# Kernel tuning notes

Measured on AMD Instinct MI355X. Metric: run time of the kernel, lower is better.

## Reference

```python
import jax, jax.numpy as jnp
import numpy as np

NUM_GROUPS = 32
EPS = 1e-6


def group_norm(x, gamma, beta):
    # x: (b, c, h, w)
    b, c, h, w = x.shape
    xg = x.reshape(b, NUM_GROUPS, c // NUM_GROUPS, h, w)
    mean = xg.mean(axis=(2, 3, 4), keepdims=True)
    var = xg.var(axis=(2, 3, 4), keepdims=True)
    xn = (xg - mean) * jax.lax.rsqrt(var + EPS)
    xn = xn.reshape(b, c, h, w)
    return xn * gamma[None, :, None, None] + beta[None, :, None, None]


def conv1x1(x, w, bias):
    # x: (b, c_in, h, w), w: (c_out, c_in) -> (b, c_out, h, w)
    return jnp.einsum('oc,bchw->bohw', w, x) + bias[None, :, None, None]


def setup_inputs() -> dict:
    key = jax.random.key(0)
    ks = jax.random.split(key, 11)
    c = 512
    x = jax.random.normal(ks[0], (4, c, 64, 64), dtype=jnp.float32)
    s = 1.0 / np.sqrt(c)
    return {
        'x': x,
        'gamma': jnp.ones((c,), jnp.float32),
        'beta': jnp.zeros((c,), jnp.float32),
        'wq': jax.random.normal(ks[1], (c, c), jnp.float32) * s,
        'bq': jax.random.normal(ks[2], (c,), jnp.float32) * 0.01,
        'wk': jax.random.normal(ks[3], (c, c), jnp.float32) * s,
        'bk': jax.random.normal(ks[4], (c,), jnp.float32) * 0.01,
        'wv': jax.random.normal(ks[5], (c, c), jnp.float32) * s,
        'bv': jax.random.normal(ks[6], (c,), jnp.float32) * s,
        'wo': jax.random.normal(ks[7], (c, c), jnp.float32) * s,
        'bo': jax.random.normal(ks[8], (c,), jnp.float32) * 0.01,
    }


def reference(x, gamma, beta, wq, bq, wk, bk, wv, bv, wo, bo):
    b, c, h, w = x.shape
    scale = c ** (-0.5)
    xn = group_norm(x, gamma, beta)
    q = conv1x1(xn, wq, bq).reshape(b, c, h * w)
    k = conv1x1(xn, wk, bk).reshape(b, c, h * w)
    v = conv1x1(xn, wv, bv).reshape(b, c, h * w)
    attn = jnp.einsum('bci,bcj->bij', q, k) * scale  # (b, hw, hw)
    attn = jax.nn.softmax(attn, axis=2)
    out = jnp.einsum('bij,bcj->bci', attn, v).reshape(b, c, h, w)
    out = conv1x1(out, wo, bo)
    return x + out
```

## Files before the change

### kernel.cpp

```cpp
#include <hip/hip_runtime.h>

typedef _Float16 f16x8 __attribute__((ext_vector_type(8)));
typedef float f32x4 __attribute__((ext_vector_type(4)));
typedef unsigned short u16;
typedef unsigned short u16x8 __attribute__((ext_vector_type(8)));

__device__ __forceinline__ u16 f2h(float f) {
  union { _Float16 h; u16 u; } v; v.h = (_Float16)f; return v.u;
}
__device__ __forceinline__ float h2f(u16 u) {
  union { _Float16 h; u16 u; } v; v.u = u; return (float)v.h;
}

__device__ __forceinline__ void gload16(const u16* g, u16* l) {
  __builtin_amdgcn_global_load_lds((const __attribute__((address_space(1))) unsigned*)g,
                                   (__attribute__((address_space(3))) unsigned*)l, 16, 0, 0);
}

__global__ void cast4_k(const float* __restrict__ a0, const float* __restrict__ a1,
                        const float* __restrict__ a2, const float* __restrict__ a3,
                        u16* __restrict__ o) {
  const float* src = blockIdx.y == 0 ? a0 : blockIdx.y == 1 ? a1 : blockIdx.y == 2 ? a2 : a3;
  int i = blockIdx.x * 256 + threadIdx.x;
  o[(size_t)blockIdx.y * 262144 + i] = f2h(src[i]);
}

__global__ void gn_k(const float* __restrict__ x, const float* __restrict__ g_,
                     const float* __restrict__ b_, u16* __restrict__ xnt) {
  const int g = blockIdx.x, b = blockIdx.y;
  const float* xb = x + ((size_t)b * 512 + g * 16) * 4096;
  u16* ob = xnt + (size_t)b * 4096 * 512 + g * 16;
  const float4* x4 = (const float4*)xb;
  float s = 0.f, ss = 0.f;
  for (int i = threadIdx.x; i < 16384; i += 256) {
    float4 v = x4[i];
    s += v.x + v.y + v.z + v.w;
    ss += v.x * v.x + v.y * v.y + v.z * v.z + v.w * v.w;
  }
  #pragma unroll
  for (int o = 32; o; o >>= 1) { s += __shfl_down(s, o); ss += __shfl_down(ss, o); }
  __shared__ float rs[4], rss[4];
  if ((threadIdx.x & 63) == 0) { rs[threadIdx.x >> 6] = s; rss[threadIdx.x >> 6] = ss; }
  __syncthreads();
  s = rs[0] + rs[1] + rs[2] + rs[3];
  ss = rss[0] + rss[1] + rss[2] + rss[3];
  const float mean = s * (1.f / 65536.f);
  const float rstd = rsqrtf(ss * (1.f / 65536.f) - mean * mean + 1e-6f);
  __shared__ float tile[16 * 257];
  const int cc_w = threadIdx.x & 15;
  const float gam = g_[g * 16 + cc_w] * rstd;
  const float bet = b_[g * 16 + cc_w] - mean * gam;
  for (int s0 = 0; s0 < 4096; s0 += 256) {
    __syncthreads();
    #pragma unroll
    for (int cc = 0; cc < 16; ++cc)
      tile[cc * 257 + threadIdx.x] = xb[(size_t)cc * 4096 + s0 + threadIdx.x];
    __syncthreads();
    #pragma unroll
    for (int it = 0; it < 16; ++it) {
      int sl = it * 16 + (threadIdx.x >> 4);
      float v = tile[cc_w * 257 + sl] * gam + bet;
      ob[(size_t)(s0 + sl) * 512 + cc_w] = f2h(v);
    }
  }
}

__global__ void softmax_k(u16* __restrict__ S) {
  const size_t ro = ((size_t)blockIdx.y * 4096 + blockIdx.x) * 4096;
  u16x8* rv = (u16x8*)(S + ro);
  const int tid = threadIdx.x;
  u16x8 h[2];
  h[0] = rv[tid];
  h[1] = rv[256 + tid];
  float v[16];
  #pragma unroll
  for (int t = 0; t < 2; ++t)
    #pragma unroll
    for (int j = 0; j < 8; ++j) v[t * 8 + j] = h2f(h[t][j]);
  float mx = -1e30f;
  #pragma unroll
  for (int i = 0; i < 16; ++i) mx = fmaxf(mx, v[i]);
  #pragma unroll
  for (int o = 32; o; o >>= 1) mx = fmaxf(mx, __shfl_down(mx, o));
  __shared__ float rm[4], rsu[4];
  if ((tid & 63) == 0) rm[tid >> 6] = mx;
  __syncthreads();
  mx = fmaxf(fmaxf(rm[0], rm[1]), fmaxf(rm[2], rm[3]));
  float sum = 0.f;
  #pragma unroll
  for (int i = 0; i < 16; ++i) { v[i] = __expf(v[i] - mx); sum += v[i]; }
  #pragma unroll
  for (int o = 32; o; o >>= 1) sum += __shfl_down(sum, o);
  if ((tid & 63) == 0) rsu[tid >> 6] = sum;
  __syncthreads();
  const float rinv = 1.f / (rsu[0] + rsu[1] + rsu[2] + rsu[3]);
  #pragma unroll
  for (int t = 0; t < 2; ++t) {
    u16x8 o8;
    #pragma unroll
    for (int j = 0; j < 8; ++j) o8[j] = f2h(v[t * 8 + j] * rinv);
    rv[t * 256 + tid] = o8;
  }
}

template<int MODE, int BM, int BN>
__global__ void gemm_k(const u16* __restrict__ A, int lda, long long sAz,
                       const u16* __restrict__ B, int ldb, long long sBz,
                       void* __restrict__ Cp_, int ldc, long long sCz,
                       int K,
                       u16* __restrict__ Cq, u16* __restrict__ Ck, u16* __restrict__ Cvv,
                       const float* __restrict__ bq, const float* __restrict__ bk,
                       const float* __restrict__ bvp) {
  const unsigned gx = gridDim.x, gy = gridDim.y;
  const unsigned lin = (blockIdx.z * gy + blockIdx.y) * gx + blockIdx.x;
  const unsigned nwg = gx * gy * gridDim.z;
  const unsigned swz = (lin & 7) * (nwg >> 3) + (lin >> 3);
  const unsigned bx = swz % gx;
  const unsigned rem = swz / gx;
  const unsigned by = rem % gy;
  const unsigned bz = rem / gy;

  constexpr int LK = 64;
  __shared__ u16 As[BM * LK];
  __shared__ u16 Bs[BN * LK];
  const int tid = threadIdx.x;
  const int m0 = by * BM;
  const int n0 = bx * BN;

  const u16* Ab;
  const u16* Bb;
  if constexpr (MODE == 5) {
    int proj = bz >> 2, b = bz & 3;
    Ab = A + (size_t)proj * 512 * 512;
    Bb = B + (size_t)b * 4096 * 512;
  } else {
    Ab = A + (size_t)bz * sAz;
    Bb = B + (size_t)bz * sBz;
  }

  constexpr int FM = BM / 32, FN = BN / 32;
  f32x4 acc[FM][FN];
  #pragma unroll
  for (int i = 0; i < FM; ++i)
    #pragma unroll
    for (int j = 0; j < FN; ++j)
      acc[i][j] = (f32x4){0.f, 0.f, 0.f, 0.f};

  const int wid = tid >> 6;
  const int lane = tid & 63;
  const int wm = (wid >> 1) * (BM / 2);
  const int wn = (wid & 1) * (BN / 2);
  const int l15 = lane & 15;
  const int lk8 = (lane >> 4) * 8;
  const int lrow = lane >> 3;
  const int lcol = (lane & 7) * 8;

  constexpr int ACH = BM / 8;
  constexpr int BCH = BN / 8;

  for (int k0 = 0; k0 < K; k0 += 64) {
    #pragma unroll
    for (int c = 0; c < ACH / 4; ++c) {
      int ch = wid * (ACH / 4) + c;
      gload16(Ab + (size_t)(m0 + ch * 8 + lrow) * lda + k0 + lcol, &As[ch * 512]);
    }
    #pragma unroll
    for (int c = 0; c < BCH / 4; ++c) {
      int ch = wid * (BCH / 4) + c;
      gload16(Bb + (size_t)(n0 + ch * 8 + lrow) * ldb + k0 + lcol, &Bs[ch * 512]);
    }
    __syncthreads();
    #pragma unroll
    for (int kk = 0; kk < 64; kk += 32) {
      f16x8 af[FM], bfr[FN];
      #pragma unroll
      for (int i = 0; i < FM; ++i)
        af[i] = *(const f16x8*)&As[(wm + i * 16 + l15) * LK + kk + lk8];
      #pragma unroll
      for (int j = 0; j < FN; ++j)
        bfr[j] = *(const f16x8*)&Bs[(wn + j * 16 + l15) * LK + kk + lk8];
      #pragma unroll
      for (int i = 0; i < FM; ++i)
        #pragma unroll
        for (int j = 0; j < FN; ++j)
          acc[i][j] = __builtin_amdgcn_mfma_f32_16x16x32_f16(af[i], bfr[j], acc[i][j], 0, 0, 0);
    }
    __syncthreads();
  }

  const int lq4 = (lane >> 4) * 4;
  if constexpr (MODE == 5) {
    int proj = bz >> 2, b = bz & 3;
    const float* bs = proj == 0 ? bq : (proj == 1 ? bk : bvp);
    u16* C = (proj == 0 ? Cq : (proj == 1 ? Ck : Cvv)) + (size_t)b * 4096 * 512;
    #pragma unroll
    for (int i = 0; i < FM; ++i) {
      int mb = m0 + wm + i * 16 + lq4;
      float b0 = bs[mb], b1 = bs[mb + 1], b2 = bs[mb + 2], b3 = bs[mb + 3];
      #pragma unroll
      for (int j = 0; j < FN; ++j) {
        int n = n0 + wn + j * 16 + l15;
        ushort4 o4;
        o4.x = f2h(acc[i][j][0] + b0); o4.y = f2h(acc[i][j][1] + b1);
        o4.z = f2h(acc[i][j][2] + b2); o4.w = f2h(acc[i][j][3] + b3);
        *(ushort4*)(C + (size_t)n * 512 + mb) = o4;
      }
    }
    return;
  }
  u16* C = (u16*)Cp_ + (size_t)bz * sCz;
  #pragma unroll
  for (int i = 0; i < FM; ++i) {
    int mb = m0 + wm + i * 16 + lq4;
    #pragma unroll
    for (int j = 0; j < FN; ++j) {
      int n = n0 + wn + j * 16 + l15;
      #pragma unroll
      for (int r = 0; r < 4; ++r)
        C[(size_t)(mb + r) * ldc + n] = f2h(acc[i][j][r]);
    }
  }
}

template<int BM, int BN, int EPI>
__global__ __launch_bounds__(512, 2)
void gemm8_k(const u16* __restrict__ A, int lda, long long sAz,
             const u16* __restrict__ B, int ldb, long long sBz,
             void* __restrict__ Cp_, int ldc, long long sCz,
             int K,
             const float* __restrict__ bias,
             const float* __restrict__ resid, long long sRz,
             float scale) {
  const unsigned gx = gridDim.x, gy = gridDim.y;
  const unsigned lin = (blockIdx.z * gy + blockIdx.y) * gx + blockIdx.x;
  const unsigned nwg = gx * gy * gridDim.z;
  const unsigned swzb = (lin & 7) * (nwg >> 3) + (lin >> 3);
  const unsigned bx = swzb % gx;
  const unsigned rem = swzb / gx;
  const unsigned by = rem % gy;
  const unsigned bz = rem / gy;

  constexpr int ACH = BM / 64;
  constexpr int BCH = BN / 64;
  constexpr int NLD = ACH + BCH;
  constexpr int HBUF = (BM + BN) * 64;
  __shared__ u16 lds[2 * HBUF];

  const int tid = threadIdx.x;
  const int m0 = by * BM;
  const int n0 = bx * BN;
  const u16* Ab = A + (size_t)bz * sAz + (size_t)m0 * lda;
  const u16* Bb = B + (size_t)bz * sBz + (size_t)n0 * ldb;

  int offA[ACH], offB[BCH];
  #pragma unroll
  for (int i = 0; i < ACH; ++i) {
    int ch = i * 512 + tid;
    int row = ch >> 3;
    int c16 = (ch & 7) ^ (row & 7);
    offA[i] = row * lda + c16 * 8;
  }
  #pragma unroll
  for (int i = 0; i < BCH; ++i) {
    int ch = i * 512 + tid;
    int row = ch >> 3;
    int c16 = (ch & 7) ^ (row & 7);
    offB[i] = row * ldb + c16 * 8;
  }

  const int wid = tid >> 6;
  const int lane = tid & 63;
  const int wm = (wid >> 2) * (BM / 2);
  const int wn = (wid & 3) * (BN / 4);
  const int l15 = lane & 15;
  const int lk8 = (lane >> 4) * 8;

  constexpr int FM = BM / 32;
  constexpr int FN = BN / 64;
  f32x4 acc[FM][FN];
  #pragma unroll
  for (int i = 0; i < FM; ++i)
    #pragma unroll
    for (int j = 0; j < FN; ++j)
      acc[i][j] = (f32x4){0.f, 0.f, 0.f, 0.f};

  const int NT = K >> 6;

  auto stage = [&](int t) {
    u16* dst = &lds[(t & 1) * HBUF];
    const u16* as = Ab + t * 64;
    #pragma unroll
    for (int i = 0; i < ACH; ++i)
      gload16(as + offA[i], dst + (i * 512 + tid) * 8);
    const u16* bs = Bb + t * 64;
    u16* dstB = dst + BM * 64;
    #pragma unroll
    for (int i = 0; i < BCH; ++i)
      gload16(bs + offB[i], dstB + (i * 512 + tid) * 8);
  };

  stage(0);
  stage(1);

  for (int t = 0; t < NT; ++t) {
    if (t < NT - 1)
      asm volatile("s_waitcnt vmcnt(%0)" :: "i"(NLD) : "memory");
    else
      asm volatile("s_waitcnt vmcnt(0)" ::: "memory");
    __builtin_amdgcn_s_barrier();
    __builtin_amdgcn_sched_barrier(0);

    const u16* Asp = &lds[(t & 1) * HBUF];
    const u16* Bsp = Asp + BM * 64;

    f16x8 bf[2][FN];
    #pragma unroll
    for (int k2 = 0; k2 < 2; ++k2)
      #pragma unroll
      for (int j = 0; j < FN; ++j) {
        int row = wn + j * 16 + l15;
        int col = (k2 * 32 + lk8) ^ ((row & 7) << 3);
        bf[k2][j] = *(const f16x8*)&Bsp[row * 64 + col];
      }
    #pragma unroll
    for (int q = 0; q < FM / 2; ++q) {
      f16x8 af[2][2];
      #pragma unroll
      for (int k2 = 0; k2 < 2; ++k2)
        #pragma unroll
        for (int s = 0; s < 2; ++s) {
          int row = wm + (2 * q + s) * 16 + l15;
          int col = (k2 * 32 + lk8) ^ ((row & 7) << 3);
          af[k2][s] = *(const f16x8*)&Asp[row * 64 + col];
        }
      __builtin_amdgcn_s_setprio(1);
      #pragma unroll
      for (int k2 = 0; k2 < 2; ++k2)
        #pragma unroll
        for (int s = 0; s < 2; ++s)
          #pragma unroll
          for (int j = 0; j < FN; ++j)
            acc[2 * q + s][j] =
                __builtin_amdgcn_mfma_f32_16x16x32_f16(af[k2][s], bf[k2][j], acc[2 * q + s][j], 0, 0, 0);
      __builtin_amdgcn_s_setprio(0);
    }

    asm volatile("s_waitcnt lgkmcnt(0)" ::: "memory");
    __builtin_amdgcn_sched_barrier(0);
    __builtin_amdgcn_s_barrier();
    if (t + 2 < NT) stage(t + 2);
  }

  const int lq4 = (lane >> 4) * 4;
  #pragma unroll
  for (int i = 0; i < FM; ++i) {
    int mb = m0 + wm + i * 16 + lq4;
    #pragma unroll
    for (int j = 0; j < FN; ++j) {
      int n = n0 + wn + j * 16 + l15;
      if constexpr (EPI == 0) {
        u16* C = (u16*)Cp_ + (size_t)bz * sCz;
        #pragma unroll
        for (int r = 0; r < 4; ++r)
          C[(size_t)(mb + r) * ldc + n] = f2h(acc[i][j][r] * scale);
      } else {
        float* C = (float*)Cp_ + (size_t)bz * sCz;
        const float* R = resid + (size_t)bz * sRz;
        #pragma unroll
        for (int r = 0; r < 4; ++r)
          C[(size_t)(mb + r) * ldc + n] = acc[i][j][r] + bias[mb + r] + R[(size_t)(mb + r) * ldc + n];
      }
    }
  }
}

extern "C" void kernel_launch(void* const* d_in, const int* in_sizes, int n_in,
                              void* d_out, int out_size, void* d_ws, size_t ws_size,
                              hipStream_t stream) {
  const float* x     = (const float*)d_in[0];
  const float* gamma = (const float*)d_in[1];
  const float* beta  = (const float*)d_in[2];
  const float* wq    = (const float*)d_in[3];
  const float* bq    = (const float*)d_in[4];
  const float* wk    = (const float*)d_in[5];
  const float* bk    = (const float*)d_in[6];
  const float* wv    = (const float*)d_in[7];
  const float* bv    = (const float*)d_in[8];
  const float* wo    = (const float*)d_in[9];
  const float* bo    = (const float*)d_in[10];
  float* out = (float*)d_out;

  const size_t BHW = (size_t)4096 * 512;
  const long long SS = 16777216LL;
  u16* Wh  = (u16*)d_ws;
  u16* xnt = Wh + (size_t)4 * 512 * 512;
  u16* qt  = xnt + 4 * BHW;
  u16* kt  = qt + 4 * BHW;
  u16* vt  = kt + 4 * BHW;
  u16* Sb  = vt + 4 * BHW;
  u16* Vp  = xnt;

  const float scale = 0.044194173824159216f;

  hipLaunchKernelGGL(cast4_k, dim3(1024, 4), dim3(256), 0, stream, wq, wk, wv, wo, Wh);
  hipLaunchKernelGGL(gn_k, dim3(32, 4), dim3(256), 0, stream, x, gamma, beta, xnt);

  hipLaunchKernelGGL((gemm_k<5, 128, 128>), dim3(32, 4, 12), dim3(256), 0, stream,
                     Wh, 512, 0LL, xnt, 512, 0LL, nullptr, 0, 0LL, 512,
                     qt, kt, vt, bq, bk, bv);

  hipLaunchKernelGGL((gemm8_k<256, 256, 0>), dim3(16, 16, 4), dim3(512), 0, stream,
                     qt, 512, (long long)BHW, kt, 512, (long long)BHW,
                     Sb, 4096, SS, 512, nullptr, nullptr, 0LL, scale);

  hipLaunchKernelGGL(softmax_k, dim3(4096, 4), dim3(256), 0, stream, Sb);

  hipLaunchKernelGGL((gemm_k<4, 128, 128>), dim3(32, 4, 4), dim3(256), 0, stream,
                     Wh + (size_t)3 * 512 * 512, 512, 0LL, vt, 512, (long long)BHW,
                     Vp, 4096, (long long)(512 * 4096), 512,
                     nullptr, nullptr, nullptr, nullptr, nullptr, nullptr);

  hipLaunchKernelGGL((gemm8_k<128, 256, 1>), dim3(16, 4, 4), dim3(512), 0, stream,
                     Vp, 4096, (long long)(512 * 4096), Sb, 4096, SS,
                     out, 4096, (long long)BHW, 4096, bo, x, (long long)BHW, 0.f);
}
```

Before: 408.5 us.

## Fuse softmax into QK^T epilogue with atomic row sums and deferred normalization

Drops the separate softmax kernel. The QK^T GEMM epilogue now exponentiates the scaled scores without subtracting a row max, clamping them to the fp16 range. It accumulates per-row sums with atomics into a zeroed buffer and stages the tile through LDS for vectorized stores. The final PV GEMM applies 1/rowsum per column in its epilogue, also through an LDS-staged coalesced path. This saves a full read and write of the 4096x4096 score matrix, but skipping the max subtraction risks overflow or precision loss for larger logits.

After: 452.6 us. 1.11x slower.

```diff
diff --git a/kernel.cpp b/kernel.cpp
--- a/kernel.cpp
+++ b/kernel.cpp
@@ -15,6 +15,10 @@
 __device__ __forceinline__ void gload16(const u16* g, u16* l) {
   __builtin_amdgcn_global_load_lds((const __attribute__((address_space(1))) unsigned*)g,
                                    (__attribute__((address_space(3))) unsigned*)l, 16, 0, 0);
+}
+
+__global__ void zero_k(float* __restrict__ p) {
+  p[blockIdx.x * 256 + threadIdx.x] = 0.f;
 }
 
 __global__ void cast4_k(const float* __restrict__ a0, const float* __restrict__ a1,
@@ -62,44 +66,6 @@
       float v = tile[cc_w * 257 + sl] * gam + bet;
       ob[(size_t)(s0 + sl) * 512 + cc_w] = f2h(v);
     }
-  }
-}
-
-__global__ void softmax_k(u16* __restrict__ S) {
-  const size_t ro = ((size_t)blockIdx.y * 4096 + blockIdx.x) * 4096;
-  u16x8* rv = (u16x8*)(S + ro);
-  const int tid = threadIdx.x;
-  u16x8 h[2];
-  h[0] = rv[tid];
-  h[1] = rv[256 + tid];
-  float v[16];
-  #pragma unroll
-  for (int t = 0; t < 2; ++t)
-    #pragma unroll
-    for (int j = 0; j < 8; ++j) v[t * 8 + j] = h2f(h[t][j]);
-  float mx = -1e30f;
-  #pragma unroll
-  for (int i = 0; i < 16; ++i) mx = fmaxf(mx, v[i]);
-  #pragma unroll
-  for (int o = 32; o; o >>= 1) mx = fmaxf(mx, __shfl_down(mx, o));
-  __shared__ float rm[4], rsu[4];
-  if ((tid & 63) == 0) rm[tid >> 6] = mx;
-  __syncthreads();
-  mx = fmaxf(fmaxf(rm[0], rm[1]), fmaxf(rm[2], rm[3]));
-  float sum = 0.f;
-  #pragma unroll
-  for (int i = 0; i < 16; ++i) { v[i] = __expf(v[i] - mx); sum += v[i]; }
-  #pragma unroll
-  for (int o = 32; o; o >>= 1) sum += __shfl_down(sum, o);
-  if ((tid & 63) == 0) rsu[tid >> 6] = sum;
-  __syncthreads();
-  const float rinv = 1.f / (rsu[0] + rsu[1] + rsu[2] + rsu[3]);
-  #pragma unroll
-  for (int t = 0; t < 2; ++t) {
-    u16x8 o8;
-    #pragma unroll
-    for (int j = 0; j < 8; ++j) o8[j] = f2h(v[t * 8 + j] * rinv);
-    rv[t * 256 + tid] = o8;
   }
 }
 
@@ -230,7 +196,7 @@
              int K,
              const float* __restrict__ bias,
              const float* __restrict__ resid, long long sRz,
-             float scale) {
+             float scale, float* __restrict__ rowsum) {
   const unsigned gx = gridDim.x, gy = gridDim.y;
   const unsigned lin = (blockIdx.z * gy + blockIdx.y) * gx + blockIdx.x;
   const unsigned nwg = gx * gy * gridDim.z;
@@ -244,7 +210,9 @@
   constexpr int BCH = BN / 64;
   constexpr int NLD = ACH + BCH;
   constexpr int HBUF = (BM + BN) * 64;
-  __shared__ u16 lds[2 * HBUF];
+  constexpr int EPIN = EPI == 1 ? BM * BN * 2 : BM * BN;
+  constexpr int LDSN = 2 * HBUF > EPIN ? 2 * HBUF : EPIN;
+  __shared__ u16 lds[LDSN];
 
   const int tid = threadIdx.x;
   const int m0 = by * BM;
@@ -352,24 +320,82 @@
   }
 
   const int lq4 = (lane >> 4) * 4;
-  #pragma unroll
-  for (int i = 0; i < FM; ++i) {
-    int mb = m0 + wm + i * 16 + lq4;
-    #pragma unroll
-    for (int j = 0; j < FN; ++j) {
-      int n = n0 + wn + j * 16 + l15;
-      if constexpr (EPI == 0) {
-        u16* C = (u16*)Cp_ + (size_t)bz * sCz;
+
+  if constexpr (EPI == 0) {
+    constexpr float L2E = 1.44269504088896f;
+    #pragma unroll
+    for (int i = 0; i < FM; ++i) {
+      #pragma unroll
+      for (int j = 0; j < FN; ++j)
         #pragma unroll
         for (int r = 0; r < 4; ++r)
-          C[(size_t)(mb + r) * ldc + n] = f2h(acc[i][j][r] * scale);
-      } else {
-        float* C = (float*)Cp_ + (size_t)bz * sCz;
-        const float* R = resid + (size_t)bz * sRz;
+          acc[i][j][r] = fminf(__builtin_amdgcn_exp2f(acc[i][j][r] * (scale * L2E)), 60000.f);
+      f32x4 rs = acc[i][0];
+      #pragma unroll
+      for (int j = 1; j < FN; ++j) rs += acc[i][j];
+      #pragma unroll
+      for (int off = 1; off < 16; off <<= 1) {
+        f32x4 o;
+        #pragma unroll
+        for (int r = 0; r < 4; ++r) o[r] = __shfl_xor(rs[r], off);
+        rs += o;
+      }
+      if (l15 == 0) {
+        int mb = m0 + wm + i * 16 + lq4;
         #pragma unroll
         for (int r = 0; r < 4; ++r)
-          C[(size_t)(mb + r) * ldc + n] = acc[i][j][r] + bias[mb + r] + R[(size_t)(mb + r) * ldc + n];
-      }
+          atomicAdd(&rowsum[(size_t)bz * 4096 + mb + r], rs[r]);
+      }
+      #pragma unroll
+      for (int j = 0; j < FN; ++j) {
+        int cc = wn + j * 16 + l15;
+        #pragma unroll
+        for (int r = 0; r < 4; ++r)
+          lds[(wm + i * 16 + lq4 + r) * BN + cc] = f2h(acc[i][j][r]);
+      }
+    }
+    __syncthreads();
+    u16* Sg = (u16*)Cp_ + (size_t)bz * sCz;
+    const int col = (tid * 8) & (BN - 1);
+    const int rw0 = (tid * 8) / BN;
+    constexpr int RPS = 512 * 8 / BN;
+    #pragma unroll
+    for (int s = 0; s < BM / RPS; ++s) {
+      int row = s * RPS + rw0;
+      *(u16x8*)(Sg + (size_t)(m0 + row) * ldc + n0 + col) =
+          *(const u16x8*)&lds[row * BN + col];
+    }
+  } else {
+    float* tf = (float*)lds;
+    #pragma unroll
+    for (int i = 0; i < FM; ++i)
+      #pragma unroll
+      for (int j = 0; j < FN; ++j) {
+        int cc = wn + j * 16 + l15;
+        #pragma unroll
+        for (int r = 0; r < 4; ++r)
+          tf[(wm + i * 16 + lq4 + r) * BN + cc] = acc[i][j][r];
+      }
+    __syncthreads();
+    float* C = (float*)Cp_ + (size_t)bz * sCz;
+    const float* R = resid + (size_t)bz * sRz;
+    const int col = (tid * 4) & (BN - 1);
+    const int rw0 = (tid * 4) / BN;
+    constexpr int RPS = 512 * 4 / BN;
+    float4 rv = *(const float4*)&rowsum[(size_t)bz * 4096 + n0 + col];
+    float4 ri;
+    ri.x = 1.f / rv.x; ri.y = 1.f / rv.y; ri.z = 1.f / rv.z; ri.w = 1.f / rv.w;
+    #pragma unroll
+    for (int s = 0; s < BM / RPS; ++s) {
+      int row = s * RPS + rw0;
+      float b = bias[m0 + row];
+      float4 v = *(const float4*)&tf[row * BN + col];
+      float4 xr = *(const float4*)(R + (size_t)(m0 + row) * ldc + n0 + col);
+      v.x = v.x * ri.x + b + xr.x;
+      v.y = v.y * ri.y + b + xr.y;
+      v.z = v.z * ri.z + b + xr.z;
+      v.w = v.w * ri.w + b + xr.w;
+      *(float4*)(C + (size_t)(m0 + row) * ldc + n0 + col) = v;
     }
   }
 }
@@ -398,10 +424,12 @@
   u16* kt  = qt + 4 * BHW;
   u16* vt  = kt + 4 * BHW;
   u16* Sb  = vt + 4 * BHW;
+  float* rowsum = (float*)(Sb + 4 * SS);
   u16* Vp  = xnt;
 
   const float scale = 0.044194173824159216f;
 
+  hipLaunchKernelGGL(zero_k, dim3(64), dim3(256), 0, stream, rowsum);
   hipLaunchKernelGGL(cast4_k, dim3(1024, 4), dim3(256), 0, stream, wq, wk, wv, wo, Wh);
   hipLaunchKernelGGL(gn_k, dim3(32, 4), dim3(256), 0, stream, x, gamma, beta, xnt);
 
@@ -411,9 +439,7 @@
 
   hipLaunchKernelGGL((gemm8_k<256, 256, 0>), dim3(16, 16, 4), dim3(512), 0, stream,
                      qt, 512, (long long)BHW, kt, 512, (long long)BHW,
-                     Sb, 4096, SS, 512, nullptr, nullptr, 0LL, scale);
-
-  hipLaunchKernelGGL(softmax_k, dim3(4096, 4), dim3(256), 0, stream, Sb);
+                     Sb, 4096, SS, 512, nullptr, nullptr, 0LL, scale, rowsum);
 
   hipLaunchKernelGGL((gemm_k<4, 128, 128>), dim3(32, 4, 4), dim3(256), 0, stream,
                      Wh + (size_t)3 * 512 * 512, 512, 0LL, vt, 512, (long long)BHW,
@@ -422,5 +448,5 @@
 
   hipLaunchKernelGGL((gemm8_k<128, 256, 1>), dim3(16, 4, 4), dim3(512), 0, stream,
                      Vp, 4096, (long long)(512 * 4096), Sb, 4096, SS,
-                     out, 4096, (long long)BHW, 4096, bo, x, (long long)BHW, 0.f);
-}
+                     out, 4096, (long long)BHW, 4096, bo, x, (long long)BHW, 0.f, rowsum);
+}
```
